# Kernel optimization log

Measured on AMD Instinct MI355X. Metric: run time of the kernel, lower is better.

Reference implementation:

```python
import jax, jax.numpy as jnp
import numpy as np

N = 50000          # nodes
E = 1600000        # edges (before self-loops)
DIN = 128
HEADS = (8, 8, 4)
FEATS = (16, 16, 16)
NEG_SLOPE = 0.2


def setup_inputs() -> dict:
    key = jax.random.key(0)
    ks = jax.random.split(key, 2 + 4 * 3)
    inp = {
        "X": jax.random.normal(ks[0], (N, DIN), dtype=jnp.float32),
        "A": jax.random.randint(ks[1], (2, E), 0, N, dtype=jnp.int32),
    }
    in_dims = [DIN, HEADS[0] * FEATS[0], HEADS[1] * FEATS[1]]
    k = 2
    for i, (h, f) in enumerate(zip(HEADS, FEATS)):
        din = in_dims[i]
        concat = i + 1 < len(HEADS)
        inp[f"W{i+1}"] = jax.random.normal(ks[k], (din, h * f), dtype=jnp.float32) / np.float32(np.sqrt(din)); k += 1
        inp[f"as{i+1}"] = jax.random.normal(ks[k], (h, f), dtype=jnp.float32) * 0.1; k += 1
        inp[f"ad{i+1}"] = jax.random.normal(ks[k], (h, f), dtype=jnp.float32) * 0.1; k += 1
        inp[f"b{i+1}"] = jnp.zeros((h * f if concat else f,), dtype=jnp.float32); k += 1
    return inp


def _gat_conv(x, src, dst, W, a_src, a_dst, b, concat):
    # PyG-style GATConv (eval mode, self-loops already in src/dst)
    H, F = a_src.shape
    h = (x @ W).reshape(-1, H, F)                     # [N, H, F]
    e = jax.nn.leaky_relu((h * a_src).sum(-1)[src] + (h * a_dst).sum(-1)[dst], NEG_SLOPE)  # [Etot, H]
    m = jax.ops.segment_max(e, dst, num_segments=N)   # segment softmax over dst neighborhoods
    ex = jnp.exp(e - m[dst])
    s = jax.ops.segment_sum(ex, dst, num_segments=N)
    alpha = ex / (s[dst] + 1e-16)                     # [Etot, H]
    out = jax.ops.segment_sum(h[src] * alpha[:, :, None], dst, num_segments=N)  # [N, H, F]
    out = out.reshape(N, H * F) if concat else out.mean(axis=1)
    return out + b


def reference(X, A, W1, as1, ad1, b1, W2, as2, ad2, b2, W3, as3, ad3, b3):
    loops = jnp.arange(N, dtype=A.dtype)              # GATConv default add_self_loops=True
    src = jnp.concatenate([A[0], loops])
    dst = jnp.concatenate([A[1], loops])
    x = jax.nn.relu(_gat_conv(X, src, dst, W1, as1, ad1, b1, True))
    x = jax.nn.relu(_gat_conv(x, src, dst, W2, as2, ad2, b2, True))
    return _gat_conv(x, src, dst, W3, as3, ad3, b3, False)
```

## Files before the change

kernel.cpp:

```cpp
#include <hip/hip_runtime.h>
#include <hip/hip_bf16.h>

#define NN 50000
#define EE 1600000
#define DIN 128

#define BKT_SHIFT 6
#define NB ((NN + 63) >> 6)
#define BSLACK 2688
#define CHUNK 4096

typedef _Float16 half_t;
typedef __attribute__((ext_vector_type(2))) _Float16 half2_t;
typedef __attribute__((ext_vector_type(4))) _Float16 half4_t;
typedef __attribute__((ext_vector_type(8))) _Float16 half8_t;
typedef __attribute__((ext_vector_type(4))) float float4_t;

__global__ __launch_bounds__(256) void prep_kernel(
    const float* __restrict__ X, const float* __restrict__ W1,
    const float* __restrict__ W2, const float* __restrict__ W3,
    half_t* __restrict__ Xh, half_t* __restrict__ Xl,
    half_t* __restrict__ B1h, half_t* __restrict__ B1l,
    half_t* __restrict__ B2h, half_t* __restrict__ B2l,
    half_t* __restrict__ B3h, half_t* __restrict__ B3l,
    int* __restrict__ gcursor) {
    int b = blockIdx.x;
    if (b < 6250) {
        int i = b * 256 + threadIdx.x;
        if (i * 4 < NN * DIN) {
            float4 xv = *(const float4*)(X + (size_t)i * 4);
            half4_t hh, ll;
            hh[0] = (half_t)xv.x; ll[0] = (half_t)(xv.x - (float)hh[0]);
            hh[1] = (half_t)xv.y; ll[1] = (half_t)(xv.y - (float)hh[1]);
            hh[2] = (half_t)xv.z; ll[2] = (half_t)(xv.z - (float)hh[2]);
            hh[3] = (half_t)xv.w; ll[3] = (half_t)(xv.w - (float)hh[3]);
            *(half4_t*)(Xh + (size_t)i * 4) = hh;
            *(half4_t*)(Xl + (size_t)i * 4) = ll;
        }
    } else if (b < 6250 + 160) {
        int id = (b - 6250) * 256 + threadIdx.x;
        if (id < 16384) {
            int kk = id >> 7, nn = id & 127;
            float v = W1[id];
            half_t h = (half_t)v;
            B1h[nn * 128 + kk] = h;
            B1l[nn * 128 + kk] = (half_t)(v - (float)h);
        } else if (id < 32768) {
            int id2 = id - 16384;
            int kk = id2 >> 7, nn = id2 & 127;
            float v = W2[id2];
            half_t h = (half_t)v;
            B2h[nn * 128 + kk] = h;
            B2l[nn * 128 + kk] = (half_t)(v - (float)h);
        } else {
            int id3 = id - 32768;
            int kk = id3 >> 6, nn = id3 & 63;
            float v = W3[id3];
            half_t h = (half_t)v;
            B3h[nn * 128 + kk] = h;
            B3l[nn * 128 + kk] = (half_t)(v - (float)h);
        }
    } else {
        int i = (b - 6410) * 256 + threadIdx.x;
        if (i < NB) gcursor[i] = 0;
    }
}

__global__ __launch_bounds__(256) void bin_kernel(const int* __restrict__ A,
                                                  int* __restrict__ gcursor,
                                                  int* __restrict__ binned, int e, int n) {
    __shared__ int lcount[NB];
    __shared__ int lbase[NB];
    int chunk0 = blockIdx.x * CHUNK;
    int cend = chunk0 + CHUNK;
    if (cend > e + n) cend = e + n;
    for (int i = threadIdx.x; i < NB; i += 256) lcount[i] = 0;
    __syncthreads();
    int sreg[16], dreg[16];
#pragma unroll
    for (int l = 0; l < 16; ++l) {
        int i = chunk0 + l * 256 + threadIdx.x;
        if (i < cend) {
            if (i < e) { sreg[l] = A[i]; dreg[l] = A[e + i]; }
            else       { sreg[l] = dreg[l] = i - e; }
            atomicAdd(&lcount[dreg[l] >> BKT_SHIFT], 1);
        } else {
            dreg[l] = -1;
        }
    }
    __syncthreads();
    for (int b = threadIdx.x; b < NB; b += 256) {
        int c = lcount[b];
        lbase[b] = c ? atomicAdd(&gcursor[b], c) : 0;
        lcount[b] = 0;
    }
    __syncthreads();
#pragma unroll
    for (int l = 0; l < 16; ++l) {
        if (dreg[l] >= 0) {
            int bkt = dreg[l] >> BKT_SHIFT;
            int pos = lbase[bkt] + atomicAdd(&lcount[bkt], 1);
            if (pos < BSLACK)
                binned[(size_t)bkt * BSLACK + pos] = (sreg[l] << 6) | (dreg[l] & 63);
        }
    }
}

__global__ __launch_bounds__(256) void fine_scatter(const int* __restrict__ binned,
                                                    const int* __restrict__ gcursor,
                                                    int* __restrict__ begE,
                                                    int* __restrict__ endE,
                                                    int* __restrict__ csr) {
    __shared__ int lc[64];
    __shared__ int scur[64];
    int b = blockIdx.x;
    int node0 = b << BKT_SHIFT;
    int cnt = gcursor[b];
    if (cnt > BSLACK) cnt = BSLACK;
    const int* bp = binned + (size_t)b * BSLACK;
    if (threadIdx.x < 64) lc[threadIdx.x] = 0;
    __syncthreads();
    for (int j = threadIdx.x; j < cnt; j += 256) atomicAdd(&lc[bp[j] & 63], 1);
    __syncthreads();
    if (threadIdx.x < 64) {
        int lane = threadIdx.x;
        int c = lc[lane];
        int v = c;
#pragma unroll
        for (int off = 1; off < 64; off <<= 1) {
            int u = __shfl_up(v, off, 64);
            if (lane >= off) v += u;
        }
        int begin = b * BSLACK + v - c;
        scur[lane] = begin;
        int node = node0 + lane;
        if (node < NN) {
            begE[node] = begin;
            endE[node] = begin + c;
        }
    }
    __syncthreads();
    for (int j = threadIdx.x; j < cnt; j += 256) {
        int v = bp[j];
        int pos = atomicAdd(&scur[v & 63], 1);
        csr[pos] = v >> 6;
    }
}

template <int NT>
__global__ __launch_bounds__(256) void gemm_mfma(
    const half_t* __restrict__ Ah, const half_t* __restrict__ Al,
    const half_t* __restrict__ Bth, const half_t* __restrict__ Btl,
    const float* __restrict__ asrc, const float* __restrict__ adst,
    half_t* __restrict__ C16, float* __restrict__ ss, float* __restrict__ ds, int M) {
    constexpr int NCOL = NT * 16;
    __shared__ __align__(16) half_t cs[4][16][NCOL + 8];
    int tid = threadIdx.x;
    int w = tid >> 6, lane = tid & 63;
    int m = lane & 15, q = lane >> 4;
    int row0 = blockIdx.x * 64 + w * 16;

    int ar = row0 + m;
    if (ar >= M) ar = M - 1;
    const half_t* pa = Ah + (size_t)ar * 128 + q * 8;
    const half_t* pl = Al + (size_t)ar * 128 + q * 8;
    half8_t ahf[4], alf[4];
#pragma unroll
    for (int k0 = 0; k0 < 4; ++k0) {
        ahf[k0] = *(const half8_t*)(pa + k0 * 32);
        alf[k0] = *(const half8_t*)(pl + k0 * 32);
    }

    float4_t acc[NT];
#pragma unroll
    for (int nt = 0; nt < NT; ++nt) {
        acc[nt][0] = 0.f; acc[nt][1] = 0.f; acc[nt][2] = 0.f; acc[nt][3] = 0.f;
    }

#pragma unroll
    for (int nt = 0; nt < NT; ++nt) {
        const half_t* pbh = Bth + (size_t)(nt * 16 + m) * 128 + q * 8;
        const half_t* pbl = Btl + (size_t)(nt * 16 + m) * 128 + q * 8;
        half8_t bh[4], bl[4];
#pragma unroll
        for (int k0 = 0; k0 < 4; ++k0) {
            bh[k0] = *(const half8_t*)(pbh + k0 * 32);
            bl[k0] = *(const half8_t*)(pbl + k0 * 32);
        }
#pragma unroll
        for (int k0 = 0; k0 < 4; ++k0) {
            acc[nt] = __builtin_amdgcn_mfma_f32_16x16x32_f16(ahf[k0], bh[k0], acc[nt], 0, 0, 0);
            acc[nt] = __builtin_amdgcn_mfma_f32_16x16x32_f16(ahf[k0], bl[k0], acc[nt], 0, 0, 0);
            acc[nt] = __builtin_amdgcn_mfma_f32_16x16x32_f16(alf[k0], bh[k0], acc[nt], 0, 0, 0);
        }
    }

    float asv[NT], adv[NT];
#pragma unroll
    for (int nt = 0; nt < NT; ++nt) {
        asv[nt] = asrc[nt * 16 + m];
        adv[nt] = adst[nt * 16 + m];
    }
#pragma unroll
    for (int nt = 0; nt < NT; ++nt) {
#pragma unroll
        for (int r = 0; r < 4; ++r) {
            float sp = acc[nt][r] * asv[nt];
            float dp = acc[nt][r] * adv[nt];
            sp += __shfl_xor(sp, 1, 64); sp += __shfl_xor(sp, 2, 64);
            sp += __shfl_xor(sp, 4, 64); sp += __shfl_xor(sp, 8, 64);
            dp += __shfl_xor(dp, 1, 64); dp += __shfl_xor(dp, 2, 64);
            dp += __shfl_xor(dp, 4, 64); dp += __shfl_xor(dp, 8, 64);
            int grow = row0 + q * 4 + r;
            if (m == 0 && grow < M) {
                ss[(size_t)grow * NT + nt] = sp;
                ds[(size_t)grow * NT + nt] = dp;
            }
        }
    }

#pragma unroll
    for (int nt = 0; nt < NT; ++nt)
#pragma unroll
        for (int r = 0; r < 4; ++r)
            cs[w][q * 4 + r][nt * 16 + m] = (half_t)acc[nt][r];
    constexpr int LPR = NCOL / 8;
    constexpr int RPP = 64 / LPR;
    constexpr int NP = 16 / RPP;
    int rid = lane / LPR, cid = lane % LPR;
#pragma unroll
    for (int p = 0; p < NP; ++p) {
        int r = p * RPP + rid;
        int grow = row0 + r;
        half8_t v = *(const half8_t*)&cs[w][r][cid * 8];
        if (grow < M) *(half8_t*)(C16 + (size_t)grow * NCOL + cid * 8) = v;
    }
}

template <int H, int F, bool MEAN, bool RELU>
__global__ __launch_bounds__(256) void aggregate_qw(
    const half_t* __restrict__ h, const float* __restrict__ ss, const float* __restrict__ dsc_arr,
    const int* __restrict__ csr, const int* __restrict__ begE, const int* __restrict__ endE,
    const float* __restrict__ bias, half_t* __restrict__ outh, half_t* __restrict__ outl,
    float* __restrict__ out, int n) {
    constexpr int HF = H * F;
    constexpr int FPL = HF / 16;
    int wave = blockIdx.x * (blockDim.x >> 6) + (threadIdx.x >> 6);
    int lane = threadIdx.x & 63;
    if (wave >= n) return;
    int q = lane >> 4, ql = lane & 15;
    int hf = ql * FPL;
    int hh = hf / F;
    float dsc = dsc_arr[wave * H + hh];
    int begin = begE[wave], end = endE[wave];

    float ssum = 0.f;
    float acc[FPL];
#pragma unroll
    for (int k = 0; k < FPL; ++k) acc[k] = 0.f;

    int j = begin + q;
    for (; j + 12 < end; j += 16) {
        int s0 = csr[j], s1 = csr[j + 4], s2 = csr[j + 8], s3 = csr[j + 12];
        float e0 = ss[s0 * H + hh], e1 = ss[s1 * H + hh];
        float e2 = ss[s2 * H + hh], e3 = ss[s3 * H + hh];
        const half_t* p0 = h + (size_t)s0 * HF + hf;
        const half_t* p1 = h + (size_t)s1 * HF + hf;
        const half_t* p2 = h + (size_t)s2 * HF + hf;
        const half_t* p3 = h + (size_t)s3 * HF + hf;
        e0 += dsc; e0 = (e0 > 0.f) ? e0 : 0.2f * e0;
        e1 += dsc; e1 = (e1 > 0.f) ? e1 : 0.2f * e1;
        e2 += dsc; e2 = (e2 > 0.f) ? e2 : 0.2f * e2;
        e3 += dsc; e3 = (e3 > 0.f) ? e3 : 0.2f * e3;
        float x0 = __expf(e0), x1 = __expf(e1), x2 = __expf(e2), x3 = __expf(e3);
        ssum += (x0 + x1) + (x2 + x3);
        if constexpr (FPL == 8) {
            half8_t t0 = *(const half8_t*)p0, t1 = *(const half8_t*)p1;
            half8_t t2 = *(const half8_t*)p2, t3 = *(const half8_t*)p3;
#pragma unroll
            for (int k = 0; k < 8; ++k) {
                acc[k] = fmaf(x0, (float)t0[k], acc[k]);
                acc[k] = fmaf(x1, (float)t1[k], acc[k]);
                acc[k] = fmaf(x2, (float)t2[k], acc[k]);
                acc[k] = fmaf(x3, (float)t3[k], acc[k]);
            }
        } else {
            half4_t t0 = *(const half4_t*)p0, t1 = *(const half4_t*)p1;
            half4_t t2 = *(const half4_t*)p2, t3 = *(const half4_t*)p3;
#pragma unroll
            for (int k = 0; k < 4; ++k) {
                acc[k] = fmaf(x0, (float)t0[k], acc[k]);
                acc[k] = fmaf(x1, (float)t1[k], acc[k]);
                acc[k] = fmaf(x2, (float)t2[k], acc[k]);
                acc[k] = fmaf(x3, (float)t3[k], acc[k]);
            }
        }
    }
    for (; j + 4 < end; j += 8) {
        int s0 = csr[j], s1 = csr[j + 4];
        float e0 = ss[s0 * H + hh], e1 = ss[s1 * H + hh];
        const half_t* p0 = h + (size_t)s0 * HF + hf;
        const half_t* p1 = h + (size_t)s1 * HF + hf;
        e0 += dsc; e0 = (e0 > 0.f) ? e0 : 0.2f * e0;
        e1 += dsc; e1 = (e1 > 0.f) ? e1 : 0.2f * e1;
        float x0 = __expf(e0), x1 = __expf(e1);
        ssum += x0 + x1;
        if constexpr (FPL == 8) {
            half8_t t0 = *(const half8_t*)p0, t1 = *(const half8_t*)p1;
#pragma unroll
            for (int k = 0; k < 8; ++k) {
                acc[k] = fmaf(x0, (float)t0[k], acc[k]);
                acc[k] = fmaf(x1, (float)t1[k], acc[k]);
            }
        } else {
            half4_t t0 = *(const half4_t*)p0, t1 = *(const half4_t*)p1;
#pragma unroll
            for (int k = 0; k < 4; ++k) {
                acc[k] = fmaf(x0, (float)t0[k], acc[k]);
                acc[k] = fmaf(x1, (float)t1[k], acc[k]);
            }
        }
    }
    for (; j < end; j += 4) {
        int s = csr[j];
        float e = ss[s * H + hh] + dsc;
        e = (e > 0.f) ? e : 0.2f * e;
        float x = __expf(e);
        ssum += x;
        const half_t* hp = h + (size_t)s * HF + hf;
        if constexpr (FPL == 8) {
            half8_t t = *(const half8_t*)hp;
#pragma unroll
            for (int k = 0; k < 8; ++k) acc[k] = fmaf(x, (float)t[k], acc[k]);
        } else {
            half4_t t = *(const half4_t*)hp;
#pragma unroll
            for (int k = 0; k < 4; ++k) acc[k] = fmaf(x, (float)t[k], acc[k]);
        }
    }

    ssum += __shfl_xor(ssum, 16, 64);
    ssum += __shfl_xor(ssum, 32, 64);
#pragma unroll
    for (int k = 0; k < FPL; ++k) {
        acc[k] += __shfl_xor(acc[k], 16, 64);
        acc[k] += __shfl_xor(acc[k], 32, 64);
    }

    float inv = 1.f / (ssum + 1e-16f);
    if constexpr (!MEAN) {
        if (lane < 32) {
            int k0 = (lane >> 4) * 4;
            int f = (lane & 15) * FPL + k0;
            float v[4];
#pragma unroll
            for (int i = 0; i < 4; ++i) {
                v[i] = acc[k0 + i] * inv + bias[f + i];
                if (RELU) v[i] = fmaxf(v[i], 0.f);
            }
            half4_t hh4, ll4;
#pragma unroll
            for (int i = 0; i < 4; ++i) {
                hh4[i] = (half_t)v[i];
                ll4[i] = (half_t)(v[i] - (float)hh4[i]);
            }
            *(half4_t*)(outh + (size_t)wave * HF + f) = hh4;
            *(half4_t*)(outl + (size_t)wave * HF + f) = ll4;
        }
    } else {
        float val[FPL];
#pragma unroll
        for (int k = 0; k < FPL; ++k) {
            val[k] = acc[k] * inv;
            val[k] += __shfl_xor(val[k], 4, 64);
            val[k] += __shfl_xor(val[k], 8, 64);
        }
        if (lane < 4) {
            float v0 = val[0] * 0.25f + bias[lane * 4 + 0];
            float v1 = val[1] * 0.25f + bias[lane * 4 + 1];
            float v2 = val[2] * 0.25f + bias[lane * 4 + 2];
            float v3 = val[3] * 0.25f + bias[lane * 4 + 3];
            *(float4*)(out + (size_t)wave * F + lane * 4) = make_float4(v0, v1, v2, v3);
        }
    }
}

extern "C" void kernel_launch(void* const* d_in, const int* in_sizes, int n_in,
                              void* d_out, int out_size, void* d_ws, size_t ws_size,
                              hipStream_t stream) {
    const float* X  = (const float*)d_in[0];
    const int*   A  = (const int*)d_in[1];
    const float* W1 = (const float*)d_in[2];
    const float* as1 = (const float*)d_in[3];
    const float* ad1 = (const float*)d_in[4];
    const float* b1  = (const float*)d_in[5];
    const float* W2 = (const float*)d_in[6];
    const float* as2 = (const float*)d_in[7];
    const float* ad2 = (const float*)d_in[8];
    const float* b2  = (const float*)d_in[9];
    const float* W3 = (const float*)d_in[10];
    const float* as3 = (const float*)d_in[11];
    const float* ad3 = (const float*)d_in[12];
    const float* b3  = (const float*)d_in[13];

    const int N = NN, E = EE;
    const int Etot = E + N;

    char* p = (char*)d_ws;
    auto take = [&](size_t bytes) {
        char* r = p;
        p += (bytes + 255) & ~(size_t)255;
        return (void*)r;
    };
    half_t* Xh    = (half_t*)take((size_t)N * 128 * 2);
    half_t* Xl    = (half_t*)take((size_t)N * 128 * 2);
    half_t* C16   = (half_t*)take((size_t)N * 128 * 2);
    half_t* o1h   = (half_t*)take((size_t)N * 128 * 2);
    half_t* o1l   = (half_t*)take((size_t)N * 128 * 2);
    float* ssb    = (float*)take((size_t)N * 8 * 4);
    float* dsb    = (float*)take((size_t)N * 8 * 4);
    int* begE     = (int*)take((size_t)N * 4);
    int* endE     = (int*)take((size_t)N * 4);
    int* gcursor  = (int*)take((size_t)NB * 4);
    int* csr      = (int*)take((size_t)NB * BSLACK * 4);
    half_t* B1h   = (half_t*)take(128 * 128 * 2);
    half_t* B1l   = (half_t*)take(128 * 128 * 2);
    half_t* B2h   = (half_t*)take(128 * 128 * 2);
    half_t* B2l   = (half_t*)take(128 * 128 * 2);
    half_t* B3h   = (half_t*)take(64 * 128 * 2);
    half_t* B3l   = (half_t*)take(64 * 128 * 2);
    int* binned   = (int*)o1h;

    prep_kernel<<<6414, 256, 0, stream>>>(X, W1, W2, W3, Xh, Xl,
                                          B1h, B1l, B2h, B2l, B3h, B3l, gcursor);
    bin_kernel<<<(Etot + CHUNK - 1) / CHUNK, 256, 0, stream>>>(A, gcursor, binned, E, N);
    fine_scatter<<<NB, 256, 0, stream>>>(binned, gcursor, begE, endE, csr);

    const int gemmRows = (N + 63) / 64;
    const int aggBlocks = (N + 3) / 4;

    gemm_mfma<8><<<gemmRows, 256, 0, stream>>>(Xh, Xl, B1h, B1l, as1, ad1, C16, ssb, dsb, N);
    aggregate_qw<8, 16, false, true>
        <<<aggBlocks, 256, 0, stream>>>(C16, ssb, dsb, csr, begE, endE, b1, o1h, o1l, nullptr, N);

    gemm_mfma<8><<<gemmRows, 256, 0, stream>>>(o1h, o1l, B2h, B2l, as2, ad2, C16, ssb, dsb, N);
    aggregate_qw<8, 16, false, true>
        <<<aggBlocks, 256, 0, stream>>>(C16, ssb, dsb, csr, begE, endE, b2, Xh, Xl, nullptr, N);

    gemm_mfma<4><<<gemmRows, 256, 0, stream>>>(Xh, Xl, B3h, B3l, as3, ad3, C16, ssb, dsb, N);
    aggregate_qw<4, 16, true, false>
        <<<aggBlocks, 256, 0, stream>>>(C16, ssb, dsb, csr, begE, endE, b3, nullptr, nullptr,
                                        (float*)d_out, N);
}
```

Before: 407.8 us.

## Fold attention vectors into GEMM weights and fuse X fp16 split into GEMM

Precomputes W·a_src and W·a_dst as extra weight columns so the GEMM produces per-head attention scores through one extra MFMA tile, replacing the shuffle reductions. It also removes the separate pass that split X into fp16 hi/lo and converts fp32 X inside the first GEMM load. This cuts a full memory pass over X and the epilogue shuffles, at the cost of an extra MFMA tile and a slightly different rounding order for the scores.

After: 398.0 us. 1.02x faster.

```diff
diff --git a/kernel.cpp b/kernel.cpp
--- a/kernel.cpp
+++ b/kernel.cpp
@@ -16,52 +16,65 @@
 typedef __attribute__((ext_vector_type(8))) _Float16 half8_t;
 typedef __attribute__((ext_vector_type(4))) float float4_t;
 
+__device__ __forceinline__ void split_write(half_t* __restrict__ bh, half_t* __restrict__ bl,
+                                            int idx, float v) {
+    half_t h = (half_t)v;
+    bh[idx] = h;
+    bl[idx] = (half_t)(v - (float)h);
+}
+
+__device__ __forceinline__ void build_bt(const float* __restrict__ W,
+                                         const float* __restrict__ as,
+                                         const float* __restrict__ ad,
+                                         half_t* __restrict__ Bh, half_t* __restrict__ Bl,
+                                         int elem, int NCOL, int H) {
+    int r = elem >> 7, k = elem & 127;
+    float v;
+    if (r < NCOL) {
+        v = W[k * NCOL + r];
+    } else {
+        int j = r - NCOL;
+        v = 0.f;
+        if (j < 8) {
+            if (j < H) {
+                float s = 0.f;
+#pragma unroll
+                for (int f = 0; f < 16; ++f) s += W[k * NCOL + j * 16 + f] * as[j * 16 + f];
+                v = s;
+            }
+        } else {
+            int hh = j - 8;
+            if (hh < H) {
+                float s = 0.f;
+#pragma unroll
+                for (int f = 0; f < 16; ++f) s += W[k * NCOL + hh * 16 + f] * ad[hh * 16 + f];
+                v = s;
+            }
+        }
+    }
+    split_write(Bh, Bl, r * 128 + k, v);
+}
+
+#define T1 (144 * 128)
+#define T3 (80 * 128)
 __global__ __launch_bounds__(256) void prep_kernel(
-    const float* __restrict__ X, const float* __restrict__ W1,
-    const float* __restrict__ W2, const float* __restrict__ W3,
-    half_t* __restrict__ Xh, half_t* __restrict__ Xl,
+    const float* __restrict__ W1, const float* __restrict__ W2, const float* __restrict__ W3,
+    const float* __restrict__ as1, const float* __restrict__ ad1,
+    const float* __restrict__ as2, const float* __restrict__ ad2,
+    const float* __restrict__ as3, const float* __restrict__ ad3,
     half_t* __restrict__ B1h, half_t* __restrict__ B1l,
     half_t* __restrict__ B2h, half_t* __restrict__ B2l,
     half_t* __restrict__ B3h, half_t* __restrict__ B3l,
     int* __restrict__ gcursor) {
-    int b = blockIdx.x;
-    if (b < 6250) {
-        int i = b * 256 + threadIdx.x;
-        if (i * 4 < NN * DIN) {
-            float4 xv = *(const float4*)(X + (size_t)i * 4);
-            half4_t hh, ll;
-            hh[0] = (half_t)xv.x; ll[0] = (half_t)(xv.x - (float)hh[0]);
-            hh[1] = (half_t)xv.y; ll[1] = (half_t)(xv.y - (float)hh[1]);
-            hh[2] = (half_t)xv.z; ll[2] = (half_t)(xv.z - (float)hh[2]);
-            hh[3] = (half_t)xv.w; ll[3] = (half_t)(xv.w - (float)hh[3]);
-            *(half4_t*)(Xh + (size_t)i * 4) = hh;
-            *(half4_t*)(Xl + (size_t)i * 4) = ll;
-        }
-    } else if (b < 6250 + 160) {
-        int id = (b - 6250) * 256 + threadIdx.x;
-        if (id < 16384) {
-            int kk = id >> 7, nn = id & 127;
-            float v = W1[id];
-            half_t h = (half_t)v;
-            B1h[nn * 128 + kk] = h;
-            B1l[nn * 128 + kk] = (half_t)(v - (float)h);
-        } else if (id < 32768) {
-            int id2 = id - 16384;
-            int kk = id2 >> 7, nn = id2 & 127;
-            float v = W2[id2];
-            half_t h = (half_t)v;
-            B2h[nn * 128 + kk] = h;
-            B2l[nn * 128 + kk] = (half_t)(v - (float)h);
-        } else {
-            int id3 = id - 32768;
-            int kk = id3 >> 6, nn = id3 & 63;
-            float v = W3[id3];
-            half_t h = (half_t)v;
-            B3h[nn * 128 + kk] = h;
-            B3l[nn * 128 + kk] = (half_t)(v - (float)h);
-        }
+    int id = blockIdx.x * 256 + threadIdx.x;
+    if (id < T1) {
+        build_bt(W1, as1, ad1, B1h, B1l, id, 128, 8);
+    } else if (id < 2 * T1) {
+        build_bt(W2, as2, ad2, B2h, B2l, id - T1, 128, 8);
+    } else if (id < 2 * T1 + T3) {
+        build_bt(W3, as3, ad3, B3h, B3l, id - 2 * T1, 64, 4);
     } else {
-        int i = (b - 6410) * 256 + threadIdx.x;
+        int i = id - (2 * T1 + T3);
         if (i < NB) gcursor[i] = 0;
     }
 }
@@ -147,13 +160,13 @@
     }
 }
 
-template <int NT>
+template <int NTC, int H, bool A32>
 __global__ __launch_bounds__(256) void gemm_mfma(
+    const float* __restrict__ X32,
     const half_t* __restrict__ Ah, const half_t* __restrict__ Al,
     const half_t* __restrict__ Bth, const half_t* __restrict__ Btl,
-    const float* __restrict__ asrc, const float* __restrict__ adst,
     half_t* __restrict__ C16, float* __restrict__ ss, float* __restrict__ ds, int M) {
-    constexpr int NCOL = NT * 16;
+    constexpr int NCOL = NTC * 16;
     __shared__ __align__(16) half_t cs[4][16][NCOL + 8];
     int tid = threadIdx.x;
     int w = tid >> 6, lane = tid & 63;
@@ -162,23 +175,39 @@
 
     int ar = row0 + m;
     if (ar >= M) ar = M - 1;
-    const half_t* pa = Ah + (size_t)ar * 128 + q * 8;
-    const half_t* pl = Al + (size_t)ar * 128 + q * 8;
     half8_t ahf[4], alf[4];
-#pragma unroll
-    for (int k0 = 0; k0 < 4; ++k0) {
-        ahf[k0] = *(const half8_t*)(pa + k0 * 32);
-        alf[k0] = *(const half8_t*)(pl + k0 * 32);
-    }
-
-    float4_t acc[NT];
-#pragma unroll
-    for (int nt = 0; nt < NT; ++nt) {
+    if constexpr (A32) {
+        const float* px = X32 + (size_t)ar * 128 + q * 8;
+#pragma unroll
+        for (int k0 = 0; k0 < 4; ++k0) {
+            float4 u0 = *(const float4*)(px + k0 * 32);
+            float4 u1 = *(const float4*)(px + k0 * 32 + 4);
+            float uv[8] = {u0.x, u0.y, u0.z, u0.w, u1.x, u1.y, u1.z, u1.w};
+#pragma unroll
+            for (int j = 0; j < 8; ++j) {
+                half_t h = (half_t)uv[j];
+                ahf[k0][j] = h;
+                alf[k0][j] = (half_t)(uv[j] - (float)h);
+            }
+        }
+    } else {
+        const half_t* pa = Ah + (size_t)ar * 128 + q * 8;
+        const half_t* pl = Al + (size_t)ar * 128 + q * 8;
+#pragma unroll
+        for (int k0 = 0; k0 < 4; ++k0) {
+            ahf[k0] = *(const half8_t*)(pa + k0 * 32);
+            alf[k0] = *(const half8_t*)(pl + k0 * 32);
+        }
+    }
+
+    float4_t acc[NTC + 1];
+#pragma unroll
+    for (int nt = 0; nt <= NTC; ++nt) {
         acc[nt][0] = 0.f; acc[nt][1] = 0.f; acc[nt][2] = 0.f; acc[nt][3] = 0.f;
     }
 
 #pragma unroll
-    for (int nt = 0; nt < NT; ++nt) {
+    for (int nt = 0; nt <= NTC; ++nt) {
         const half_t* pbh = Bth + (size_t)(nt * 16 + m) * 128 + q * 8;
         const half_t* pbl = Btl + (size_t)(nt * 16 + m) * 128 + q * 8;
         half8_t bh[4], bl[4];
@@ -195,32 +224,18 @@
         }
     }
 
-    float asv[NT], adv[NT];
-#pragma unroll
-    for (int nt = 0; nt < NT; ++nt) {
-        asv[nt] = asrc[nt * 16 + m];
-        adv[nt] = adst[nt * 16 + m];
-    }
-#pragma unroll
-    for (int nt = 0; nt < NT; ++nt) {
-#pragma unroll
-        for (int r = 0; r < 4; ++r) {
-            float sp = acc[nt][r] * asv[nt];
-            float dp = acc[nt][r] * adv[nt];
-            sp += __shfl_xor(sp, 1, 64); sp += __shfl_xor(sp, 2, 64);
-            sp += __shfl_xor(sp, 4, 64); sp += __shfl_xor(sp, 8, 64);
-            dp += __shfl_xor(dp, 1, 64); dp += __shfl_xor(dp, 2, 64);
-            dp += __shfl_xor(dp, 4, 64); dp += __shfl_xor(dp, 8, 64);
-            int grow = row0 + q * 4 + r;
-            if (m == 0 && grow < M) {
-                ss[(size_t)grow * NT + nt] = sp;
-                ds[(size_t)grow * NT + nt] = dp;
-            }
-        }
-    }
-
-#pragma unroll
-    for (int nt = 0; nt < NT; ++nt)
+#pragma unroll
+    for (int r = 0; r < 4; ++r) {
+        int grow = row0 + q * 4 + r;
+        if (grow < M) {
+            float v = acc[NTC][r];
+            if (m < H) ss[(size_t)grow * H + m] = v;
+            else if (m >= 8 && m < 8 + H) ds[(size_t)grow * H + (m - 8)] = v;
+        }
+    }
+
+#pragma unroll
+    for (int nt = 0; nt < NTC; ++nt)
 #pragma unroll
         for (int r = 0; r < 4; ++r)
             cs[w][q * 4 + r][nt * 16 + m] = (half_t)acc[nt][r];
@@ -412,42 +427,45 @@
         p += (bytes + 255) & ~(size_t)255;
         return (void*)r;
     };
-    half_t* Xh    = (half_t*)take((size_t)N * 128 * 2);
-    half_t* Xl    = (half_t*)take((size_t)N * 128 * 2);
     half_t* C16   = (half_t*)take((size_t)N * 128 * 2);
-    half_t* o1h   = (half_t*)take((size_t)N * 128 * 2);
-    half_t* o1l   = (half_t*)take((size_t)N * 128 * 2);
+    half_t* Ph    = (half_t*)take((size_t)N * 128 * 2);
+    half_t* Pl    = (half_t*)take((size_t)N * 128 * 2);
     float* ssb    = (float*)take((size_t)N * 8 * 4);
     float* dsb    = (float*)take((size_t)N * 8 * 4);
     int* begE     = (int*)take((size_t)N * 4);
     int* endE     = (int*)take((size_t)N * 4);
     int* gcursor  = (int*)take((size_t)NB * 4);
     int* csr      = (int*)take((size_t)NB * BSLACK * 4);
-    half_t* B1h   = (half_t*)take(128 * 128 * 2);
-    half_t* B1l   = (half_t*)take(128 * 128 * 2);
-    half_t* B2h   = (half_t*)take(128 * 128 * 2);
-    half_t* B2l   = (half_t*)take(128 * 128 * 2);
-    half_t* B3h   = (half_t*)take(64 * 128 * 2);
-    half_t* B3l   = (half_t*)take(64 * 128 * 2);
-    int* binned   = (int*)o1h;
-
-    prep_kernel<<<6414, 256, 0, stream>>>(X, W1, W2, W3, Xh, Xl,
-                                          B1h, B1l, B2h, B2l, B3h, B3l, gcursor);
+    half_t* B1h   = (half_t*)take(144 * 128 * 2);
+    half_t* B1l   = (half_t*)take(144 * 128 * 2);
+    half_t* B2h   = (half_t*)take(144 * 128 * 2);
+    half_t* B2l   = (half_t*)take(144 * 128 * 2);
+    half_t* B3h   = (half_t*)take(80 * 128 * 2);
+    half_t* B3l   = (half_t*)take(80 * 128 * 2);
+    int* binned   = (int*)Ph;
+
+    const int prepTotal = 2 * T1 + T3 + NB;
+    prep_kernel<<<(prepTotal + 255) / 256, 256, 0, stream>>>(
+        W1, W2, W3, as1, ad1, as2, ad2, as3, ad3,
+        B1h, B1l, B2h, B2l, B3h, B3l, gcursor);
     bin_kernel<<<(Etot + CHUNK - 1) / CHUNK, 256, 0, stream>>>(A, gcursor, binned, E, N);
     fine_scatter<<<NB, 256, 0, stream>>>(binned, gcursor, begE, endE, csr);
 
     const int gemmRows = (N + 63) / 64;
     const int aggBlocks = (N + 3) / 4;
 
-    gemm_mfma<8><<<gemmRows, 256, 0, stream>>>(Xh, Xl, B1h, B1l, as1, ad1, C16, ssb, dsb, N);
+    gemm_mfma<8, 8, true><<<gemmRows, 256, 0, stream>>>(X, nullptr, nullptr,
+                                                        B1h, B1l, C16, ssb, dsb, N);
     aggregate_qw<8, 16, false, true>
-        <<<aggBlocks, 256, 0, stream>>>(C16, ssb, dsb, csr, begE, endE, b1, o1h, o1l, nullptr, N);
-
-    gemm_mfma<8><<<gemmRows, 256, 0, stream>>>(o1h, o1l, B2h, B2l, as2, ad2, C16, ssb, dsb, N);
+        <<<aggBlocks, 256, 0, stream>>>(C16, ssb, dsb, csr, begE, endE, b1, Ph, Pl, nullptr, N);
+
+    gemm_mfma<8, 8, false><<<gemmRows, 256, 0, stream>>>(nullptr, Ph, Pl,
+                                                         B2h, B2l, C16, ssb, dsb, N);
     aggregate_qw<8, 16, false, true>
-        <<<aggBlocks, 256, 0, stream>>>(C16, ssb, dsb, csr, begE, endE, b2, Xh, Xl, nullptr, N);
-
-    gemm_mfma<4><<<gemmRows, 256, 0, stream>>>(Xh, Xl, B3h, B3l, as3, ad3, C16, ssb, dsb, N);
+        <<<aggBlocks, 256, 0, stream>>>(C16, ssb, dsb, csr, begE, endE, b2, Ph, Pl, nullptr, N);
+
+    gemm_mfma<4, 4, false><<<gemmRows, 256, 0, stream>>>(nullptr, Ph, Pl,
+                                                         B3h, B3l, C16, ssb, dsb, N);
     aggregate_qw<4, 16, true, false>
         <<<aggBlocks, 256, 0, stream>>>(C16, ssb, dsb, csr, begE, endE, b3, nullptr, nullptr,
                                         (float*)d_out, N);
```
